# Performance work log

Hardware: AMD Instinct MI355X
Metric: run time of the kernel (lower is better)

Reference implementation:

```python
import jax, jax.numpy as jnp
import numpy as np

NEG_SLOPE = 0.2
EPS = 1e-16  # PyG softmax eps


def _gat_conv(x, src, dst, W, att_src, att_dst, bias, heads, out_ch):
    """PyG GATConv (eval mode, self-loops already appended, concat output)."""
    N = x.shape[0]
    xw = (x @ W).reshape(N, heads, out_ch)            # [N,H,C]
    a_src = jnp.sum(xw * att_src, axis=-1)            # [N,H]
    a_dst = jnp.sum(xw * att_dst, axis=-1)            # [N,H]
    e = jax.nn.leaky_relu(a_src[src] + a_dst[dst], NEG_SLOPE)  # [E,H]
    m = jax.ops.segment_max(e, dst, num_segments=N)   # [N,H] (self-loops -> no empty segs)
    e = jnp.exp(e - m[dst])
    denom = jax.ops.segment_sum(e, dst, num_segments=N)
    alpha = e / (denom[dst] + EPS)                    # [E,H]
    msg = xw[src] * alpha[:, :, None]                 # [E,H,C]
    out = jax.ops.segment_sum(msg, dst, num_segments=N)  # [N,H,C]
    return out.reshape(N, heads * out_ch) + bias


def setup_inputs() -> dict:
    key = jax.random.key(0)
    ks = jax.random.split(key, 12)
    N, E, F_in, H, C, NC = 20000, 320000, 512, 8, 64, 32
    x = jax.random.normal(ks[0], (N, F_in), dtype=jnp.float32)
    edge_index = jax.random.randint(ks[1], (2, E), 0, N, dtype=jnp.int64)
    g = lambda k, shape, fan: jax.random.normal(k, shape, dtype=jnp.float32) * (1.0 / np.sqrt(fan))
    return {
        "x": x,
        "edge_index": edge_index,
        "W1": g(ks[2], (F_in, H * C), F_in),
        "att_src1": g(ks[3], (H, C), C),
        "att_dst1": g(ks[4], (H, C), C),
        "b1": jnp.zeros((H * C,), dtype=jnp.float32),
        "W2": g(ks[5], (H * C, NC), H * C),
        "att_src2": g(ks[6], (1, NC), NC),
        "att_dst2": g(ks[7], (1, NC), NC),
        "b2": jnp.zeros((NC,), dtype=jnp.float32),
    }


def reference(x, edge_index, W1, att_src1, att_dst1, b1, W2, att_src2, att_dst2, b2):
    N = x.shape[0]
    H, C = att_src1.shape
    NC = att_src2.shape[1]
    # GATConv adds self-loops by default
    loops = jnp.arange(N, dtype=edge_index.dtype)
    src = jnp.concatenate([edge_index[0], loops])
    dst = jnp.concatenate([edge_index[1], loops])
    h = _gat_conv(x, src, dst, W1, att_src1, att_dst1, b1, H, C)
    h = jax.nn.elu(h)
    h = _gat_conv(h, src, dst, W2, att_src2, att_dst2, b2, 1, NC)
    return jax.nn.log_softmax(h, axis=1)
```

## Files before the change

kernel.cpp:

```cpp
#include <hip/hip_runtime.h>
#include <math.h>

#define NEG_SLOPE 0.2f
#define SM_EPS 1e-16f

typedef short short8 __attribute__((ext_vector_type(8)));
typedef float floatx4 __attribute__((ext_vector_type(4)));


__device__ inline unsigned short f2bf(float x) {
    unsigned int u = __float_as_uint(x);
    unsigned int r = (u + 0x7FFFu + ((u >> 16) & 1u)) >> 16;
    return (unsigned short)r;
}

__device__ inline float bf2f(unsigned short h) {
    return __uint_as_float(((unsigned int)h) << 16);
}

__device__ inline float bflo(unsigned int u) { return __uint_as_float(u << 16); }
__device__ inline float bfhi(unsigned int u) { return __uint_as_float(u & 0xFFFF0000u); }

__device__ inline float2 bf2x2(unsigned int u) {
    return make_float2(__uint_as_float(u << 16), __uint_as_float(u & 0xFFFF0000u));
}
__device__ inline float2 pk_fma(float w, float2 v, float2 a) {
    return make_float2(fmaf(w, v.x, a.x), fmaf(w, v.y, a.y));
}

__device__ __forceinline__ void gl_lds16(const unsigned short* g, unsigned short* l) {
    __builtin_amdgcn_global_load_lds(
        (const __attribute__((address_space(1))) unsigned int*)(g),
        (__attribute__((address_space(3))) unsigned int*)(l), 16, 0, 0);
}

__device__ inline void get_edge(const int* __restrict__ srcA, const int* __restrict__ dstA,
                                int e, int E, int& s, int& d) {
    if (e < E) { s = srcA[e]; d = dstA[e]; }
    else { s = e - E; d = e - E; }
}


__global__ __launch_bounds__(256) void k_prep(const float* __restrict__ x,
                                              unsigned short* __restrict__ xb,
                                              const float* __restrict__ W1,
                                              unsigned short* __restrict__ w1t,
                                              const float* __restrict__ W2,
                                              unsigned short* __restrict__ w2bt,
                                              const int* __restrict__ dstA,
                                              int E, int Ep,
                                              int* __restrict__ deg,
                                              int nblk_deg, int nblk_x) {
    __shared__ float tile[32][33];
    int bx = blockIdx.x;
    int t = threadIdx.x;
    if (bx < nblk_deg) {
        int e = bx * 256 + t;
        if (e < Ep) {
            int d = (e < E) ? dstA[e] : (e - E);
            atomicAdd(&deg[d], 1);
        }
    } else if (bx < nblk_deg + nblk_x) {
        int i = ((bx - nblk_deg) * 256 + t) * 4;
        float4 v = *(const float4*)(x + i);
        ushort4 o;
        o.x = f2bf(v.x); o.y = f2bf(v.y); o.z = f2bf(v.z); o.w = f2bf(v.w);
        *(ushort4*)(xb + i) = o;
    } else if (bx < nblk_deg + nblk_x + 256) {
        int b = bx - nblk_deg - nblk_x;
        int kb = (b & 15) * 32;
        int nb = (b >> 4) * 32;
        int tx = t & 31, ty = t >> 5;
        #pragma unroll
        for (int i = 0; i < 32; i += 8)
            tile[ty + i][tx] = W1[(size_t)(kb + ty + i) * 512 + nb + tx];
        __syncthreads();
        #pragma unroll
        for (int i = 0; i < 32; i += 8)
            w1t[(size_t)(nb + ty + i) * 512 + kb + tx] = f2bf(tile[tx][ty + i]);
    } else {
        int i = (bx - nblk_deg - nblk_x - 256) * 256 + t;
        int c = i >> 9, k = i & 511;
        w2bt[i] = f2bf(W2[k * 32 + c]);
    }
}


__global__ __launch_bounds__(256) void k_scan_fused(const int* __restrict__ deg,
                                                    int* __restrict__ part,
                                                    int* __restrict__ done,
                                                    int* __restrict__ off,
                                                    int* __restrict__ cursor,
                                                    int N, int nblk) {
    __shared__ int sm[256];
    int bx = blockIdx.x, t = threadIdx.x;
    int i = bx * 256 + t;
    int v = (i < N) ? deg[i] : 0;
    sm[t] = v; __syncthreads();
    for (int o = 1; o < 256; o <<= 1) {
        int x = (t >= o) ? sm[t - o] : 0;
        __syncthreads();
        sm[t] += x;
        __syncthreads();
    }
    int incl_v = sm[t];
    if (t == 255) {
        part[bx] = sm[255];
        __threadfence();
        atomicAdd(done, 1);
    }
    if (t == 0) {
        while (atomicAdd(done, 0) < nblk) { }
        __threadfence();
    }
    __syncthreads();
    int partial = 0;
    for (int j = t; j < bx; j += 256) partial += atomicAdd(&part[j], 0);
    sm[t] = partial; __syncthreads();
    for (int o = 128; o > 0; o >>= 1) {
        if (t < o) sm[t] += sm[t + o];
        __syncthreads();
    }
    int base = sm[0];
    if (i < N) {
        int vv = incl_v + base;
        off[i + 1] = vv;
        cursor[i] = vv - v;
        if (i == 0) off[0] = 0;
    }
}

__global__ __launch_bounds__(256) void k_scatter(const int* __restrict__ srcA, const int* __restrict__ dstA,
                                                 int E, int Ep, int* __restrict__ cursor,
                                                 int* __restrict__ src_s) {
    int e = blockIdx.x * 256 + threadIdx.x;
    if (e >= Ep) return;
    int s, d; get_edge(srcA, dstA, e, E, s, d);
    int p = atomicAdd(&cursor[d], 1);
    src_s[p] = s;
}


__global__ __launch_bounds__(256, 4) void k_gemm1_mfma(const unsigned short* __restrict__ A,
                                                       const unsigned short* __restrict__ Bt,
                                                       const float* __restrict__ att_s,
                                                       const float* __restrict__ att_d,
                                                       unsigned short* __restrict__ C,
                                                       float* __restrict__ a_sd,
                                                       float* __restrict__ a_dd, int M) {
    const int K = 512;
    __shared__ unsigned short As[2][64 * 32];
    __shared__ unsigned short Bs[2][128 * 32];
    int t = threadIdx.x;
    int lane = t & 63;
    int w = t >> 6;
    int row0 = blockIdx.x * 64;
    int col0 = blockIdx.y * 128;
    int wm = (w >> 1) * 32, wn = (w & 1) * 64;
    int l15 = lane & 15, q = lane >> 4;

    int srl = lane >> 2;
    int sgc = ((lane & 3) ^ ((lane >> 3) & 3)) * 8;

    floatx4 acc[2][4] = {};

    auto STAGE = [&](int buf, int k0) {
        gl_lds16(A  + (size_t)(row0 + w * 16 + srl) * K + k0 + sgc, &As[buf][(w * 16) * 32]);
        gl_lds16(Bt + (size_t)(col0 + w * 32 + srl) * K + k0 + sgc, &Bs[buf][(w * 32) * 32]);
        gl_lds16(Bt + (size_t)(col0 + w * 32 + 16 + srl) * K + k0 + sgc, &Bs[buf][(w * 32 + 16) * 32]);
    };

    STAGE(0, 0);
    asm volatile("s_waitcnt vmcnt(0)" ::: "memory");
    __builtin_amdgcn_s_barrier();

    int swz = (l15 >> 1) & 3;
    int buf = 0;
    for (int k0 = 0; k0 < K; k0 += 32) {
        if (k0 + 32 < K) {
            STAGE(buf ^ 1, k0 + 32);
            asm volatile("s_waitcnt vmcnt(3)" ::: "memory");
        } else {
            asm volatile("s_waitcnt vmcnt(0)" ::: "memory");
        }
        __builtin_amdgcn_s_barrier();
        __builtin_amdgcn_sched_barrier(0);
        short8 af[2], bfr[4];
        int sw = (q ^ swz) << 3;
        #pragma unroll
        for (int i = 0; i < 2; ++i)
            af[i] = *(const short8*)(&As[buf][(wm + i * 16 + l15) * 32 + sw]);
        #pragma unroll
        for (int j = 0; j < 4; ++j)
            bfr[j] = *(const short8*)(&Bs[buf][(wn + j * 16 + l15) * 32 + sw]);
        #pragma unroll
        for (int i = 0; i < 2; ++i)
            #pragma unroll
            for (int j = 0; j < 4; ++j)
                acc[i][j] = __builtin_amdgcn_mfma_f32_16x16x32_bf16(af[i], bfr[j], acc[i][j], 0, 0, 0);
        asm volatile("s_waitcnt lgkmcnt(0)" ::: "memory");
        __builtin_amdgcn_sched_barrier(0);
        __builtin_amdgcn_s_barrier();
        buf ^= 1;
    }

    #pragma unroll
    for (int i = 0; i < 2; ++i) {
        #pragma unroll
        for (int p = 0; p < 4; ++p) {
            int r = row0 + wm + i * 16 + q * 4 + p;
            if (r < M) {
                #pragma unroll
                for (int j = 0; j < 4; ++j) {
                    int c = col0 + wn + j * 16 + l15;
                    C[(size_t)r * 512 + c] = f2bf(acc[i][j][p]);
                }
            }
        }
    }

    int hh = blockIdx.y * 2 + (w & 1);
    float asr[4], adr[4];
    #pragma unroll
    for (int j = 0; j < 4; ++j) {
        asr[j] = att_s[hh * 64 + j * 16 + l15];
        adr[j] = att_d[hh * 64 + j * 16 + l15];
    }
    #pragma unroll
    for (int i = 0; i < 2; ++i) {
        #pragma unroll
        for (int p = 0; p < 4; ++p) {
            float ds = 0.f, dd = 0.f;
            #pragma unroll
            for (int j = 0; j < 4; ++j) {
                ds = fmaf(acc[i][j][p], asr[j], ds);
                dd = fmaf(acc[i][j][p], adr[j], dd);
            }
            #pragma unroll
            for (int mk = 1; mk <= 8; mk <<= 1) {
                ds += __shfl_xor(ds, mk);
                dd += __shfl_xor(dd, mk);
            }
            int r = row0 + wm + i * 16 + q * 4 + p;
            if (l15 == 0 && r < M) {
                a_sd[(size_t)hh * M + r] = ds;
                a_dd[(size_t)hh * M + r] = dd;
            }
        }
    }
}


__global__ __launch_bounds__(256) void k_l1(const unsigned short* __restrict__ xw,
                                            const float* __restrict__ a_s,
                                            const float* __restrict__ a_d,
                                            const int* __restrict__ off,
                                            const int* __restrict__ src_s,
                                            const float* __restrict__ bias,
                                            unsigned short* __restrict__ hout, int N) {
    int wid = threadIdx.x >> 6, lane = threadIdx.x & 63;
    int h = blockIdx.x & 7;
    int n = (blockIdx.x >> 3) * 32 + wid * 8 + (lane >> 3);
    int li = lane & 7;
    if (n >= N) return;
    int p0 = off[n], p1 = off[n + 1];
    const float* ash = a_s + (size_t)h * N;
    float adv = a_d[(size_t)h * N + n];
    const size_t cbase = (size_t)h * 64 + (size_t)li * 8;

    float2 acc[4] = {};
    float s = 0.f;
    int p = p0;
    if (p + 4 <= p1) {
        int s0 = src_s[p], s1 = src_s[p + 1], s2 = src_s[p + 2], s3 = src_s[p + 3];
        while (true) {
            const uint4 u0 = *(const uint4*)(xw + (size_t)s0 * 512 + cbase);
            const uint4 u1 = *(const uint4*)(xw + (size_t)s1 * 512 + cbase);
            const uint4 u2 = *(const uint4*)(xw + (size_t)s2 * 512 + cbase);
            const uint4 u3 = *(const uint4*)(xw + (size_t)s3 * 512 + cbase);
            float e0 = ash[s0] + adv; e0 = e0 > 0.f ? e0 : NEG_SLOPE * e0;
            float e1 = ash[s1] + adv; e1 = e1 > 0.f ? e1 : NEG_SLOPE * e1;
            float e2 = ash[s2] + adv; e2 = e2 > 0.f ? e2 : NEG_SLOPE * e2;
            float e3 = ash[s3] + adv; e3 = e3 > 0.f ? e3 : NEG_SLOPE * e3;
            int np = p + 4;
            bool more = (np + 4 <= p1);
            int t0 = 0, t1 = 0, t2 = 0, t3 = 0;
            if (more) {
                t0 = src_s[np]; t1 = src_s[np + 1];
                t2 = src_s[np + 2]; t3 = src_s[np + 3];
            }
            float w0 = __expf(e0);
            float w1 = __expf(e1);
            float w2 = __expf(e2);
            float w3 = __expf(e3);
            s += (w0 + w1) + (w2 + w3);
            acc[0] = pk_fma(w0, bf2x2(u0.x), acc[0]);
            acc[1] = pk_fma(w0, bf2x2(u0.y), acc[1]);
            acc[2] = pk_fma(w0, bf2x2(u0.z), acc[2]);
            acc[3] = pk_fma(w0, bf2x2(u0.w), acc[3]);
            acc[0] = pk_fma(w1, bf2x2(u1.x), acc[0]);
            acc[1] = pk_fma(w1, bf2x2(u1.y), acc[1]);
            acc[2] = pk_fma(w1, bf2x2(u1.z), acc[2]);
            acc[3] = pk_fma(w1, bf2x2(u1.w), acc[3]);
            acc[0] = pk_fma(w2, bf2x2(u2.x), acc[0]);
            acc[1] = pk_fma(w2, bf2x2(u2.y), acc[1]);
            acc[2] = pk_fma(w2, bf2x2(u2.z), acc[2]);
            acc[3] = pk_fma(w2, bf2x2(u2.w), acc[3]);
            acc[0] = pk_fma(w3, bf2x2(u3.x), acc[0]);
            acc[1] = pk_fma(w3, bf2x2(u3.y), acc[1]);
            acc[2] = pk_fma(w3, bf2x2(u3.z), acc[2]);
            acc[3] = pk_fma(w3, bf2x2(u3.w), acc[3]);
            p = np;
            if (!more) break;
            s0 = t0; s1 = t1; s2 = t2; s3 = t3;
        }
    }
    for (; p < p1; ++p) {
        int s0 = src_s[p];
        const uint4 u0 = *(const uint4*)(xw + (size_t)s0 * 512 + cbase);
        float e0 = ash[s0] + adv; e0 = e0 > 0.f ? e0 : NEG_SLOPE * e0;
        float w0 = __expf(e0);
        s += w0;
        acc[0] = pk_fma(w0, bf2x2(u0.x), acc[0]);
        acc[1] = pk_fma(w0, bf2x2(u0.y), acc[1]);
        acc[2] = pk_fma(w0, bf2x2(u0.z), acc[2]);
        acc[3] = pk_fma(w0, bf2x2(u0.w), acc[3]);
    }

    float inv = 1.f / (s + SM_EPS);
    unsigned int ov[4];
    #pragma unroll
    for (int j = 0; j < 4; ++j) {
        float v0 = acc[j].x * inv + bias[cbase + 2 * j];
        float v1 = acc[j].y * inv + bias[cbase + 2 * j + 1];
        v0 = v0 > 0.f ? v0 : __expf(v0) - 1.f;
        v1 = v1 > 0.f ? v1 : __expf(v1) - 1.f;
        ov[j] = (unsigned int)f2bf(v0) | ((unsigned int)f2bf(v1) << 16);
    }
    *(uint4*)(hout + (size_t)n * 512 + cbase) = make_uint4(ov[0], ov[1], ov[2], ov[3]);
}


__global__ __launch_bounds__(256) void k_gemm2_mfma(const unsigned short* __restrict__ A,
                                                    const unsigned short* __restrict__ Bt,
                                                    const float* __restrict__ att_s,
                                                    const float* __restrict__ att_d,
                                                    unsigned short* __restrict__ O,
                                                    float* __restrict__ a_s, float* __restrict__ a_d,
                                                    int M) {
    const int K = 512;
    __shared__ unsigned short As[64 * 512];
    __shared__ unsigned short Bs[32 * 512];
    int t = threadIdx.x;
    int lane = t & 63;
    int w = t >> 6;
    int row0 = blockIdx.x * 64;
    int l15 = lane & 15, q = lane >> 4;

    #pragma unroll
    for (int i = 0; i < 16; ++i) {
        int r = w * 16 + i;
        gl_lds16(A + (size_t)(row0 + r) * K + ((lane ^ (r & 7)) << 3), &As[r * 512]);
    }
    #pragma unroll
    for (int i = 0; i < 8; ++i) {
        int r = w * 8 + i;
        gl_lds16(Bt + (size_t)r * K + ((lane ^ (r & 7)) << 3), &Bs[r * 512]);
    }
    __syncthreads();

    floatx4 acc[2] = {};
    int ra = w * 16 + l15;
    int rb0 = l15, rb1 = 16 + l15;
    #pragma unroll
    for (int k0 = 0; k0 < K; k0 += 32) {
        int cc = (k0 >> 3) + q;
        short8 af = *(const short8*)(&As[ra * 512 + ((cc ^ (ra & 7)) << 3)]);
        short8 b0 = *(const short8*)(&Bs[rb0 * 512 + ((cc ^ (rb0 & 7)) << 3)]);
        short8 b1 = *(const short8*)(&Bs[rb1 * 512 + ((cc ^ (rb1 & 7)) << 3)]);
        acc[0] = __builtin_amdgcn_mfma_f32_16x16x32_bf16(af, b0, acc[0], 0, 0, 0);
        acc[1] = __builtin_amdgcn_mfma_f32_16x16x32_bf16(af, b1, acc[1], 0, 0, 0);
    }

    float as_lo = att_s[l15], as_hi = att_s[16 + l15];
    float ad_lo = att_d[l15], ad_hi = att_d[16 + l15];
    #pragma unroll
    for (int p = 0; p < 4; ++p) {
        int r = row0 + w * 16 + q * 4 + p;
        bool ok = r < M;
        float v0 = acc[0][p], v1 = acc[1][p];
        if (ok) {
            O[(size_t)r * 32 + l15]      = f2bf(v0);
            O[(size_t)r * 32 + 16 + l15] = f2bf(v1);
        }
        float ds = v0 * as_lo + v1 * as_hi;
        float dd = v0 * ad_lo + v1 * ad_hi;
        #pragma unroll
        for (int mk = 1; mk <= 8; mk <<= 1) {
            ds += __shfl_xor(ds, mk);
            dd += __shfl_xor(dd, mk);
        }
        if (ok && l15 == 0) { a_s[r] = ds; a_d[r] = dd; }
    }
}


__global__ __launch_bounds__(256) void k_l2(const unsigned short* __restrict__ hw2,
                                            const float* __restrict__ a_s,
                                            const float* __restrict__ a_d,
                                            const int* __restrict__ off,
                                            const int* __restrict__ src_s,
                                            const float* __restrict__ bias,
                                            float* __restrict__ outp, int N) {
    int wid = threadIdx.x >> 6, lane = threadIdx.x & 63;
    int n = blockIdx.x * 4 + wid;
    if (n >= N) return;
    int p0 = off[n], p1 = off[n + 1];
    float adv = a_d[n];
    int e8 = lane >> 3;
    int li = lane & 7;
    const int cbase = li * 4;

    float acc[4] = {};
    float s = 0.f;
    int p = p0;
    for (; p + 16 <= p1; p += 16) {
        int sA = src_s[p + e8];
        int sB = src_s[p + 8 + e8];
        const uint2 uA = *(const uint2*)(hw2 + (size_t)sA * 32 + cbase);
        const uint2 uB = *(const uint2*)(hw2 + (size_t)sB * 32 + cbase);
        float eA = a_s[sA] + adv; eA = eA > 0.f ? eA : NEG_SLOPE * eA;
        float eB = a_s[sB] + adv; eB = eB > 0.f ? eB : NEG_SLOPE * eB;
        float wA = __expf(eA);
        float wB = __expf(eB);
        s += wA + wB;
        acc[0] = fmaf(wA, bflo(uA.x), acc[0]); acc[1] = fmaf(wA, bfhi(uA.x), acc[1]);
        acc[2] = fmaf(wA, bflo(uA.y), acc[2]); acc[3] = fmaf(wA, bfhi(uA.y), acc[3]);
        acc[0] = fmaf(wB, bflo(uB.x), acc[0]); acc[1] = fmaf(wB, bfhi(uB.x), acc[1]);
        acc[2] = fmaf(wB, bflo(uB.y), acc[2]); acc[3] = fmaf(wB, bfhi(uB.y), acc[3]);
    }
    for (; p + 8 <= p1; p += 8) {
        int sA = src_s[p + e8];
        const uint2 uA = *(const uint2*)(hw2 + (size_t)sA * 32 + cbase);
        float eA = a_s[sA] + adv; eA = eA > 0.f ? eA : NEG_SLOPE * eA;
        float wA = __expf(eA);
        s += wA;
        acc[0] = fmaf(wA, bflo(uA.x), acc[0]); acc[1] = fmaf(wA, bfhi(uA.x), acc[1]);
        acc[2] = fmaf(wA, bflo(uA.y), acc[2]); acc[3] = fmaf(wA, bfhi(uA.y), acc[3]);
    }
    if (p < p1) {
        int nb = p1 - p;
        bool val = e8 < nb;
        int sA = src_s[val ? p + e8 : p];
        const uint2 uA = *(const uint2*)(hw2 + (size_t)sA * 32 + cbase);
        float eA = a_s[sA] + adv; eA = eA > 0.f ? eA : NEG_SLOPE * eA;
        float wA = val ? __expf(eA) : 0.f;
        s += wA;
        acc[0] = fmaf(wA, bflo(uA.x), acc[0]); acc[1] = fmaf(wA, bfhi(uA.x), acc[1]);
        acc[2] = fmaf(wA, bflo(uA.y), acc[2]); acc[3] = fmaf(wA, bfhi(uA.y), acc[3]);
    }

    #pragma unroll
    for (int mk = 8; mk <= 32; mk <<= 1) {
        s += __shfl_xor(s, mk);
        #pragma unroll
        for (int j = 0; j < 4; ++j) acc[j] += __shfl_xor(acc[j], mk);
    }

    float inv = 1.f / (s + SM_EPS);
    float v[4];
    #pragma unroll
    for (int j = 0; j < 4; ++j) v[j] = acc[j] * inv + bias[cbase + j];

    float mx = fmaxf(fmaxf(v[0], v[1]), fmaxf(v[2], v[3]));
    mx = fmaxf(mx, __shfl_xor(mx, 1));
    mx = fmaxf(mx, __shfl_xor(mx, 2));
    mx = fmaxf(mx, __shfl_xor(mx, 4));
    float sum = 0.f;
    #pragma unroll
    for (int j = 0; j < 4; ++j) sum += __expf(v[j] - mx);
    sum += __shfl_xor(sum, 1);
    sum += __shfl_xor(sum, 2);
    sum += __shfl_xor(sum, 4);
    float lse = __logf(sum);
    if (e8 == 0) {
        float4 o = make_float4(v[0] - mx - lse, v[1] - mx - lse,
                               v[2] - mx - lse, v[3] - mx - lse);
        *(float4*)(outp + (size_t)n * 32 + cbase) = o;
    }
}


extern "C" void kernel_launch(void* const* d_in, const int* in_sizes, int n_in,
                              void* d_out, int out_size, void* d_ws, size_t ws_size,
                              hipStream_t stream) {
    const float* x   = (const float*)d_in[0];
    const int*   ei  = (const int*)d_in[1];
    const float* W1  = (const float*)d_in[2];
    const float* as1 = (const float*)d_in[3];
    const float* ad1 = (const float*)d_in[4];
    const float* b1  = (const float*)d_in[5];
    const float* W2  = (const float*)d_in[6];
    const float* as2 = (const float*)d_in[7];
    const float* ad2 = (const float*)d_in[8];
    const float* b2  = (const float*)d_in[9];
    float* out = (float*)d_out;

    const int F = 512;
    const int N = in_sizes[0] / F;
    const int E = in_sizes[1] / 2;
    const int Ep = E + N;
    const int* srcA = ei;
    const int* dstA = ei + E;

    char* w = (char*)d_ws;
    auto alloc = [&](size_t b) -> void* {
        void* p = (void*)w;
        w += (b + 255) & ~(size_t)255;
        return p;
    };
    unsigned short* xbf  = (unsigned short*)alloc((size_t)N * 512 * 2);
    unsigned short* w1t  = (unsigned short*)alloc((size_t)512 * 512 * 2);
    unsigned short* w2bt = (unsigned short*)alloc((size_t)32 * 512 * 2);
    unsigned short* xw1  = (unsigned short*)alloc((size_t)N * 512 * 2);
    unsigned short* hbuf = (unsigned short*)alloc((size_t)N * 512 * 2);
    float* a_s1 = (float*)alloc((size_t)N * 8 * 4);
    float* a_d1 = (float*)alloc((size_t)N * 8 * 4);
    unsigned short* hw2 = (unsigned short*)alloc((size_t)N * 32 * 2);
    float* a_s2 = (float*)alloc((size_t)N * 4);
    float* a_d2 = (float*)alloc((size_t)N * 4);
    int* deg    = (int*)alloc((size_t)N * 4);
    int* done   = (int*)alloc(256);
    int* incl   = (int*)alloc((size_t)N * 4);
    int* part   = (int*)alloc(256 * 4);
    int* off    = (int*)alloc((size_t)(N + 1) * 4);
    int* cursor = (int*)alloc((size_t)N * 4);
    int* src_s  = (int*)alloc((size_t)Ep * 4);
    (void)incl;

    int egrid = (Ep + 255) / 256;
    int sgrid = (N + 255) / 256;
    int ngrid4 = (N + 3) / 4;
    int nblk_x = (N * 512 / 4) / 256;
    int nblk_w2 = (32 * 512 + 255) / 256;

    hipMemsetAsync(deg, 0, (((size_t)N * 4 + 255) & ~(size_t)255) + 256, stream);

    k_prep<<<egrid + nblk_x + 256 + nblk_w2, 256, 0, stream>>>(
        x, xbf, W1, w1t, W2, w2bt, dstA, E, Ep, deg, egrid, nblk_x);

    k_scan_fused<<<sgrid, 256, 0, stream>>>(deg, part, done, off, cursor, N, sgrid);
    k_scatter<<<egrid, 256, 0, stream>>>(srcA, dstA, E, Ep, cursor, src_s);

    {
        dim3 g1((N + 63) / 64, 512 / 128);
        k_gemm1_mfma<<<g1, 256, 0, stream>>>(xbf, w1t, as1, ad1, xw1, a_s1, a_d1, N);
    }
    {
        int ngrid32 = (N + 31) / 32;
        k_l1<<<ngrid32 * 8, 256, 0, stream>>>(xw1, a_s1, a_d1, off, src_s, b1, hbuf, N);
    }

    k_gemm2_mfma<<<(N + 63) / 64, 256, 0, stream>>>(hbuf, w2bt, as2, ad2, hw2, a_s2, a_d2, N);
    k_l2<<<ngrid4, 256, 0, stream>>>(hw2, a_s2, a_d2, off, src_s, b2, out, N);
}
```

Measured before the change: 222.1 us.

## Precompute layer-1 edge softmax weights in scatter, store fp16 xw, byte-offset indices

The CSR scatter kernel now runs after GEMM1 and computes exp(leaky_relu(a_s+a_d)) for all 8 heads per edge into a sorted weight buffer. The layer-1 aggregation then streams these weights instead of gathering a_s per source and evaluating exp. Source indices are stored pre-shifted as byte offsets so both aggregation kernels skip the multiply. The GEMM1 output switches from bf16 to fp16 for extra mantissa precision. In exchange, the scatter now does 16 random gathers per edge and writes an extra Ep*8 float buffer, and fp16 can overflow on large activations.

```diff
diff --git a/kernel.cpp b/kernel.cpp
--- a/kernel.cpp
+++ b/kernel.cpp
@@ -1,4 +1,5 @@
 #include <hip/hip_runtime.h>
+#include <hip/hip_fp16.h>
 #include <math.h>
 
 #define NEG_SLOPE 0.2f
@@ -21,11 +22,13 @@
 __device__ inline float bflo(unsigned int u) { return __uint_as_float(u << 16); }
 __device__ inline float bfhi(unsigned int u) { return __uint_as_float(u & 0xFFFF0000u); }
 
-__device__ inline float2 bf2x2(unsigned int u) {
-    return make_float2(__uint_as_float(u << 16), __uint_as_float(u & 0xFFFF0000u));
-}
-__device__ inline float2 pk_fma(float w, float2 v, float2 a) {
-    return make_float2(fmaf(w, v.x, a.x), fmaf(w, v.y, a.y));
+__device__ inline void fma8h(float w, const uint4& u, float2 acc[4]) {
+    const __half2* hp = reinterpret_cast<const __half2*>(&u);
+    #pragma unroll
+    for (int k = 0; k < 4; ++k) {
+        acc[k].x = fmaf(w, __half2float(__low2half(hp[k])), acc[k].x);
+        acc[k].y = fmaf(w, __half2float(__high2half(hp[k])), acc[k].y);
+    }
 }
 
 __device__ __forceinline__ void gl_lds16(const unsigned short* g, unsigned short* l) {
@@ -130,14 +133,26 @@
     }
 }
 
-__global__ __launch_bounds__(256) void k_scatter(const int* __restrict__ srcA, const int* __restrict__ dstA,
-                                                 int E, int Ep, int* __restrict__ cursor,
-                                                 int* __restrict__ src_s) {
+
+__global__ __launch_bounds__(256) void k_scatterw(const int* __restrict__ srcA,
+                                                  const int* __restrict__ dstA,
+                                                  int E, int Ep, int N,
+                                                  int* __restrict__ cursor,
+                                                  int* __restrict__ src_b,
+                                                  const float* __restrict__ a_s1,
+                                                  const float* __restrict__ a_d1,
+                                                  float* __restrict__ wbuf) {
     int e = blockIdx.x * 256 + threadIdx.x;
     if (e >= Ep) return;
     int s, d; get_edge(srcA, dstA, e, E, s, d);
     int p = atomicAdd(&cursor[d], 1);
-    src_s[p] = s;
+    src_b[p] = s << 10;
+    #pragma unroll
+    for (int h = 0; h < 8; ++h) {
+        float ev = a_s1[(size_t)h * N + s] + a_d1[(size_t)h * N + d];
+        ev = ev > 0.f ? ev : NEG_SLOPE * ev;
+        wbuf[(size_t)h * Ep + p] = __expf(ev);
+    }
 }
 
 
@@ -213,18 +228,19 @@
                 #pragma unroll
                 for (int j = 0; j < 4; ++j) {
                     int c = col0 + wn + j * 16 + l15;
-                    C[(size_t)r * 512 + c] = f2bf(acc[i][j][p]);
+                    __half hh = __float2half(acc[i][j][p]);
+                    C[(size_t)r * 512 + c] = reinterpret_cast<unsigned short&>(hh);
                 }
             }
         }
     }
 
-    int hh = blockIdx.y * 2 + (w & 1);
+    int hh2 = blockIdx.y * 2 + (w & 1);
     float asr[4], adr[4];
     #pragma unroll
     for (int j = 0; j < 4; ++j) {
-        asr[j] = att_s[hh * 64 + j * 16 + l15];
-        adr[j] = att_d[hh * 64 + j * 16 + l15];
+        asr[j] = att_s[hh2 * 64 + j * 16 + l15];
+        adr[j] = att_d[hh2 * 64 + j * 16 + l15];
     }
     #pragma unroll
     for (int i = 0; i < 2; ++i) {
@@ -243,8 +259,8 @@
             }
             int r = row0 + wm + i * 16 + q * 4 + p;
             if (l15 == 0 && r < M) {
-                a_sd[(size_t)hh * M + r] = ds;
-                a_dd[(size_t)hh * M + r] = dd;
+                a_sd[(size_t)hh2 * M + r] = ds;
+                a_dd[(size_t)hh2 * M + r] = dd;
             }
         }
     }
@@ -252,79 +268,56 @@
 
 
 __global__ __launch_bounds__(256) void k_l1(const unsigned short* __restrict__ xw,
-                                            const float* __restrict__ a_s,
-                                            const float* __restrict__ a_d,
+                                            const float* __restrict__ wbuf,
                                             const int* __restrict__ off,
-                                            const int* __restrict__ src_s,
+                                            const int* __restrict__ src_b,
                                             const float* __restrict__ bias,
-                                            unsigned short* __restrict__ hout, int N) {
+                                            unsigned short* __restrict__ hout,
+                                            int N, int Ep) {
     int wid = threadIdx.x >> 6, lane = threadIdx.x & 63;
     int h = blockIdx.x & 7;
     int n = (blockIdx.x >> 3) * 32 + wid * 8 + (lane >> 3);
     int li = lane & 7;
     if (n >= N) return;
     int p0 = off[n], p1 = off[n + 1];
-    const float* ash = a_s + (size_t)h * N;
-    float adv = a_d[(size_t)h * N + n];
+    const float* wh = wbuf + (size_t)h * Ep;
+    const char* xbase = (const char*)xw + h * 128 + li * 16;
     const size_t cbase = (size_t)h * 64 + (size_t)li * 8;
 
     float2 acc[4] = {};
     float s = 0.f;
     int p = p0;
     if (p + 4 <= p1) {
-        int s0 = src_s[p], s1 = src_s[p + 1], s2 = src_s[p + 2], s3 = src_s[p + 3];
+        int o0 = src_b[p], o1 = src_b[p + 1], o2 = src_b[p + 2], o3 = src_b[p + 3];
         while (true) {
-            const uint4 u0 = *(const uint4*)(xw + (size_t)s0 * 512 + cbase);
-            const uint4 u1 = *(const uint4*)(xw + (size_t)s1 * 512 + cbase);
-            const uint4 u2 = *(const uint4*)(xw + (size_t)s2 * 512 + cbase);
-            const uint4 u3 = *(const uint4*)(xw + (size_t)s3 * 512 + cbase);
-            float e0 = ash[s0] + adv; e0 = e0 > 0.f ? e0 : NEG_SLOPE * e0;
-            float e1 = ash[s1] + adv; e1 = e1 > 0.f ? e1 : NEG_SLOPE * e1;
-            float e2 = ash[s2] + adv; e2 = e2 > 0.f ? e2 : NEG_SLOPE * e2;
-            float e3 = ash[s3] + adv; e3 = e3 > 0.f ? e3 : NEG_SLOPE * e3;
+            const uint4 u0 = *(const uint4*)(xbase + o0);
+            const uint4 u1 = *(const uint4*)(xbase + o1);
+            const uint4 u2 = *(const uint4*)(xbase + o2);
+            const uint4 u3 = *(const uint4*)(xbase + o3);
+            float w0 = wh[p], w1 = wh[p + 1], w2 = wh[p + 2], w3 = wh[p + 3];
             int np = p + 4;
             bool more = (np + 4 <= p1);
             int t0 = 0, t1 = 0, t2 = 0, t3 = 0;
             if (more) {
-                t0 = src_s[np]; t1 = src_s[np + 1];
-                t2 = src_s[np + 2]; t3 = src_s[np + 3];
+                t0 = src_b[np]; t1 = src_b[np + 1];
+                t2 = src_b[np + 2]; t3 = src_b[np + 3];
             }
-            float w0 = __expf(e0);
-            float w1 = __expf(e1);
-            float w2 = __expf(e2);
-            float w3 = __expf(e3);
             s += (w0 + w1) + (w2 + w3);
-            acc[0] = pk_fma(w0, bf2x2(u0.x), acc[0]);
-            acc[1] = pk_fma(w0, bf2x2(u0.y), acc[1]);
-            acc[2] = pk_fma(w0, bf2x2(u0.z), acc[2]);
-            acc[3] = pk_fma(w0, bf2x2(u0.w), acc[3]);
-            acc[0] = pk_fma(w1, bf2x2(u1.x), acc[0]);
-            acc[1] = pk_fma(w1, bf2x2(u1.y), acc[1]);
-            acc[2] = pk_fma(w1, bf2x2(u1.z), acc[2]);
-            acc[3] = pk_fma(w1, bf2x2(u1.w), acc[3]);
-            acc[0] = pk_fma(w2, bf2x2(u2.x), acc[0]);
-            acc[1] = pk_fma(w2, bf2x2(u2.y), acc[1]);
-            acc[2] = pk_fma(w2, bf2x2(u2.z), acc[2]);
-            acc[3] = pk_fma(w2, bf2x2(u2.w), acc[3]);
-            acc[0] = pk_fma(w3, bf2x2(u3.x), acc[0]);
-            acc[1] = pk_fma(w3, bf2x2(u3.y), acc[1]);
-            acc[2] = pk_fma(w3, bf2x2(u3.z), acc[2]);
-            acc[3] = pk_fma(w3, bf2x2(u3.w), acc[3]);
+            fma8h(w0, u0, acc);
+            fma8h(w1, u1, acc);
+            fma8h(w2, u2, acc);
+            fma8h(w3, u3, acc);
             p = np;
             if (!more) break;
-            s0 = t0; s1 = t1; s2 = t2; s3 = t3;
+            o0 = t0; o1 = t1; o2 = t2; o3 = t3;
         }
     }
     for (; p < p1; ++p) {
-        int s0 = src_s[p];
-        const uint4 u0 = *(const uint4*)(xw + (size_t)s0 * 512 + cbase);
-        float e0 = ash[s0] + adv; e0 = e0 > 0.f ? e0 : NEG_SLOPE * e0;
-        float w0 = __expf(e0);
+        int o0 = src_b[p];
+        const uint4 u0 = *(const uint4*)(xbase + o0);
+        float w0 = wh[p];
         s += w0;
-        acc[0] = pk_fma(w0, bf2x2(u0.x), acc[0]);
-        acc[1] = pk_fma(w0, bf2x2(u0.y), acc[1]);
-        acc[2] = pk_fma(w0, bf2x2(u0.z), acc[2]);
-        acc[3] = pk_fma(w0, bf2x2(u0.w), acc[3]);
+        fma8h(w0, u0, acc);
     }
 
     float inv = 1.f / (s + SM_EPS);
@@ -409,7 +402,7 @@
                                             const float* __restrict__ a_s,
                                             const float* __restrict__ a_d,
                                             const int* __restrict__ off,
-                                            const int* __restrict__ src_s,
+                                            const int* __restrict__ src_b,
                                             const float* __restrict__ bias,
                                             float* __restrict__ outp, int N) {
     int wid = threadIdx.x >> 6, lane = threadIdx.x & 63;
@@ -420,17 +413,19 @@
     int e8 = lane >> 3;
     int li = lane & 7;
     const int cbase = li * 4;
+    const char* hb = (const char*)hw2 + cbase * 2;
+    const char* ab = (const char*)a_s;
 
     float acc[4] = {};
     float s = 0.f;
     int p = p0;
     for (; p + 16 <= p1; p += 16) {
-        int sA = src_s[p + e8];
-        int sB = src_s[p + 8 + e8];
-        const uint2 uA = *(const uint2*)(hw2 + (size_t)sA * 32 + cbase);
-        const uint2 uB = *(const uint2*)(hw2 + (size_t)sB * 32 + cbase);
-        float eA = a_s[sA] + adv; eA = eA > 0.f ? eA : NEG_SLOPE * eA;
-        float eB = a_s[sB] + adv; eB = eB > 0.f ? eB : NEG_SLOPE * eB;
+        int oA = src_b[p + e8];
+        int oB = src_b[p + 8 + e8];
+        const uint2 uA = *(const uint2*)(hb + (oA >> 4));
+        const uint2 uB = *(const uint2*)(hb + (oB >> 4));
+        float eA = *(const float*)(ab + (oA >> 8)) + adv; eA = eA > 0.f ? eA : NEG_SLOPE * eA;
+        float eB = *(const float*)(ab + (oB >> 8)) + adv; eB = eB > 0.f ? eB : NEG_SLOPE * eB;
         float wA = __expf(eA);
         float wB = __expf(eB);
         s += wA + wB;
@@ -440,9 +435,9 @@
         acc[2] = fmaf(wB, bflo(uB.y), acc[2]); acc[3] = fmaf(wB, bfhi(uB.y), acc[3]);
     }
     for (; p + 8 <= p1; p += 8) {
-        int sA = src_s[p + e8];
-        const uint2 uA = *(const uint2*)(hw2 + (size_t)sA * 32 + cbase);
-        float eA = a_s[sA] + adv; eA = eA > 0.f ? eA : NEG_SLOPE * eA;
+        int oA = src_b[p + e8];
+        const uint2 uA = *(const uint2*)(hb + (oA >> 4));
+        float eA = *(const float*)(ab + (oA >> 8)) + adv; eA = eA > 0.f ? eA : NEG_SLOPE * eA;
         float wA = __expf(eA);
         s += wA;
         acc[0] = fmaf(wA, bflo(uA.x), acc[0]); acc[1] = fmaf(wA, bfhi(uA.x), acc[1]);
@@ -451,9 +446,9 @@
     if (p < p1) {
         int nb = p1 - p;
         bool val = e8 < nb;
-        int sA = src_s[val ? p + e8 : p];
-        const uint2 uA = *(const uint2*)(hw2 + (size_t)sA * 32 + cbase);
-        float eA = a_s[sA] + adv; eA = eA > 0.f ? eA : NEG_SLOPE * eA;
+        int oA = src_b[val ? p + e8 : p];
+        const uint2 uA = *(const uint2*)(hb + (oA >> 4));
+        float eA = *(const float*)(ab + (oA >> 8)) + adv; eA = eA > 0.f ? eA : NEG_SLOPE * eA;
         float wA = val ? __expf(eA) : 0.f;
         s += wA;
         acc[0] = fmaf(wA, bflo(uA.x), acc[0]); acc[1] = fmaf(wA, bfhi(uA.x), acc[1]);
@@ -531,12 +526,11 @@
     float* a_d2 = (float*)alloc((size_t)N * 4);
     int* deg    = (int*)alloc((size_t)N * 4);
     int* done   = (int*)alloc(256);
-    int* incl   = (int*)alloc((size_t)N * 4);
     int* part   = (int*)alloc(256 * 4);
     int* off    = (int*)alloc((size_t)(N + 1) * 4);
     int* cursor = (int*)alloc((size_t)N * 4);
-    int* src_s  = (int*)alloc((size_t)Ep * 4);
-    (void)incl;
+    int* src_b  = (int*)alloc((size_t)Ep * 4);
+    float* wbuf = (float*)alloc((size_t)Ep * 8 * 4);
 
     int egrid = (Ep + 255) / 256;
     int sgrid = (N + 255) / 256;
@@ -549,18 +543,20 @@
     k_prep<<<egrid + nblk_x + 256 + nblk_w2, 256, 0, stream>>>(
         x, xbf, W1, w1t, W2, w2bt, dstA, E, Ep, deg, egrid, nblk_x);
 
-    k_scan_fused<<<sgrid, 256, 0, stream>>>(deg, part, done, off, cursor, N, sgrid);
-    k_scatter<<<egrid, 256, 0, stream>>>(srcA, dstA, E, Ep, cursor, src_s);
-
     {
         dim3 g1((N + 63) / 64, 512 / 128);
         k_gemm1_mfma<<<g1, 256, 0, stream>>>(xbf, w1t, as1, ad1, xw1, a_s1, a_d1, N);
     }
+
+    k_scan_fused<<<sgrid, 256, 0, stream>>>(deg, part, done, off, cursor, N, sgrid);
+    k_scatterw<<<egrid, 256, 0, stream>>>(srcA, dstA, E, Ep, N, cursor, src_b,
+                                          a_s1, a_d1, wbuf);
+
     {
         int ngrid32 = (N + 31) / 32;
-        k_l1<<<ngrid32 * 8, 256, 0, stream>>>(xw1, a_s1, a_d1, off, src_s, b1, hbuf, N);
+        k_l1<<<ngrid32 * 8, 256, 0, stream>>>(xw1, wbuf, off, src_b, b1, hbuf, N, Ep);
     }
 
     k_gemm2_mfma<<<(N + 63) / 64, 256, 0, stream>>>(hbuf, w2bt, as2, ad2, hw2, a_s2, a_d2, N);
-    k_l2<<<ngrid4, 256, 0, stream>>>(hw2, a_s2, a_d2, off, src_s, b2, out, N);
-}
+    k_l2<<<ngrid4, 256, 0, stream>>>(hw2, a_s2, a_d2, off, src_b, b2, out, N);
+}
```

Measured after the change: 254.3 us. +14.5%, slower.

## Enlarge layer-1 GEMM tile to 128x128 with 64-wide K steps and XOR swizzle

Applied to the files above, without the earlier changes.

Retiles the first-layer bf16 MFMA GEMM from 64x128 to 128x128 block tiles. K advances 64 per stage, each wave holds a 4x4 accumulator grid, and the LDS layout uses a new 8-way XOR swizzle. The goal is more operand reuse per LDS load and fewer barriers per K pass. In exchange it uses more LDS and registers, drops the occupancy hint, and waits for the prefetch only at the end of each step, which may weaken overlap. An unused workspace allocation is also removed.

```diff
diff --git a/kernel.cpp b/kernel.cpp
--- a/kernel.cpp
+++ b/kernel.cpp
@@ -141,71 +141,69 @@
 }
 
 
-__global__ __launch_bounds__(256, 4) void k_gemm1_mfma(const unsigned short* __restrict__ A,
-                                                       const unsigned short* __restrict__ Bt,
-                                                       const float* __restrict__ att_s,
-                                                       const float* __restrict__ att_d,
-                                                       unsigned short* __restrict__ C,
-                                                       float* __restrict__ a_sd,
-                                                       float* __restrict__ a_dd, int M) {
+__global__ __launch_bounds__(256) void k_gemm1_mfma(const unsigned short* __restrict__ A,
+                                                    const unsigned short* __restrict__ Bt,
+                                                    const float* __restrict__ att_s,
+                                                    const float* __restrict__ att_d,
+                                                    unsigned short* __restrict__ C,
+                                                    float* __restrict__ a_sd,
+                                                    float* __restrict__ a_dd, int M) {
     const int K = 512;
-    __shared__ unsigned short As[2][64 * 32];
-    __shared__ unsigned short Bs[2][128 * 32];
+    __shared__ unsigned short As[2][128 * 64];
+    __shared__ unsigned short Bs[2][128 * 64];
     int t = threadIdx.x;
     int lane = t & 63;
     int w = t >> 6;
-    int row0 = blockIdx.x * 64;
+    int row0 = blockIdx.x * 128;
     int col0 = blockIdx.y * 128;
-    int wm = (w >> 1) * 32, wn = (w & 1) * 64;
+    int wm = (w >> 1) * 64, wn = (w & 1) * 64;
     int l15 = lane & 15, q = lane >> 4;
 
-    int srl = lane >> 2;
-    int sgc = ((lane & 3) ^ ((lane >> 3) & 3)) * 8;
-
-    floatx4 acc[2][4] = {};
+    int r8 = lane >> 3;
+    int sgc = ((lane & 7) ^ r8) * 8;
+    int srow = w * 32 + r8;
+
+    floatx4 acc[4][4] = {};
 
     auto STAGE = [&](int buf, int k0) {
-        gl_lds16(A  + (size_t)(row0 + w * 16 + srl) * K + k0 + sgc, &As[buf][(w * 16) * 32]);
-        gl_lds16(Bt + (size_t)(col0 + w * 32 + srl) * K + k0 + sgc, &Bs[buf][(w * 32) * 32]);
-        gl_lds16(Bt + (size_t)(col0 + w * 32 + 16 + srl) * K + k0 + sgc, &Bs[buf][(w * 32 + 16) * 32]);
+        #pragma unroll
+        for (int i = 0; i < 4; ++i) {
+            gl_lds16(A  + (size_t)(row0 + srow + i * 8) * K + k0 + sgc, &As[buf][(w * 32 + i * 8) * 64]);
+            gl_lds16(Bt + (size_t)(col0 + srow + i * 8) * K + k0 + sgc, &Bs[buf][(w * 32 + i * 8) * 64]);
+        }
     };
 
     STAGE(0, 0);
     asm volatile("s_waitcnt vmcnt(0)" ::: "memory");
     __builtin_amdgcn_s_barrier();
 
-    int swz = (l15 >> 1) & 3;
     int buf = 0;
-    for (int k0 = 0; k0 < K; k0 += 32) {
-        if (k0 + 32 < K) {
-            STAGE(buf ^ 1, k0 + 32);
-            asm volatile("s_waitcnt vmcnt(3)" ::: "memory");
-        } else {
-            asm volatile("s_waitcnt vmcnt(0)" ::: "memory");
-        }
-        __builtin_amdgcn_s_barrier();
-        __builtin_amdgcn_sched_barrier(0);
-        short8 af[2], bfr[4];
-        int sw = (q ^ swz) << 3;
-        #pragma unroll
-        for (int i = 0; i < 2; ++i)
-            af[i] = *(const short8*)(&As[buf][(wm + i * 16 + l15) * 32 + sw]);
-        #pragma unroll
-        for (int j = 0; j < 4; ++j)
-            bfr[j] = *(const short8*)(&Bs[buf][(wn + j * 16 + l15) * 32 + sw]);
-        #pragma unroll
-        for (int i = 0; i < 2; ++i)
+    for (int k0 = 0; k0 < K; k0 += 64) {
+        if (k0 + 64 < K) STAGE(buf ^ 1, k0 + 64);
+        #pragma unroll
+        for (int ks = 0; ks < 2; ++ks) {
+            short8 af[4], bfr[4];
+            int sw = (((ks * 4 + q) ^ (l15 & 7))) * 8;
+            #pragma unroll
+            for (int i = 0; i < 4; ++i)
+                af[i] = *(const short8*)(&As[buf][(wm + i * 16 + l15) * 64 + sw]);
             #pragma unroll
             for (int j = 0; j < 4; ++j)
-                acc[i][j] = __builtin_amdgcn_mfma_f32_16x16x32_bf16(af[i], bfr[j], acc[i][j], 0, 0, 0);
-        asm volatile("s_waitcnt lgkmcnt(0)" ::: "memory");
+                bfr[j] = *(const short8*)(&Bs[buf][(wn + j * 16 + l15) * 64 + sw]);
+            #pragma unroll
+            for (int i = 0; i < 4; ++i)
+                #pragma unroll
+                for (int j = 0; j < 4; ++j)
+                    acc[i][j] = __builtin_amdgcn_mfma_f32_16x16x32_bf16(af[i], bfr[j], acc[i][j], 0, 0, 0);
+        }
+        asm volatile("s_waitcnt vmcnt(0) lgkmcnt(0)" ::: "memory");
         __builtin_amdgcn_sched_barrier(0);
         __builtin_amdgcn_s_barrier();
         buf ^= 1;
     }
 
     #pragma unroll
-    for (int i = 0; i < 2; ++i) {
+    for (int i = 0; i < 4; ++i) {
         #pragma unroll
         for (int p = 0; p < 4; ++p) {
             int r = row0 + wm + i * 16 + q * 4 + p;
@@ -227,7 +225,7 @@
         adr[j] = att_d[hh * 64 + j * 16 + l15];
     }
     #pragma unroll
-    for (int i = 0; i < 2; ++i) {
+    for (int i = 0; i < 4; ++i) {
         #pragma unroll
         for (int p = 0; p < 4; ++p) {
             float ds = 0.f, dd = 0.f;
@@ -531,12 +529,10 @@
     float* a_d2 = (float*)alloc((size_t)N * 4);
     int* deg    = (int*)alloc((size_t)N * 4);
     int* done   = (int*)alloc(256);
-    int* incl   = (int*)alloc((size_t)N * 4);
     int* part   = (int*)alloc(256 * 4);
     int* off    = (int*)alloc((size_t)(N + 1) * 4);
     int* cursor = (int*)alloc((size_t)N * 4);
     int* src_s  = (int*)alloc((size_t)Ep * 4);
-    (void)incl;
 
     int egrid = (Ep + 255) / 256;
     int sgrid = (N + 255) / 256;
@@ -553,7 +549,7 @@
     k_scatter<<<egrid, 256, 0, stream>>>(srcA, dstA, E, Ep, cursor, src_s);
 
     {
-        dim3 g1((N + 63) / 64, 512 / 128);
+        dim3 g1((N + 127) / 128, 512 / 128);
         k_gemm1_mfma<<<g1, 256, 0, stream>>>(xbf, w1t, as1, ad1, xw1, a_s1, a_d1, N);
     }
     {
```

Result: slower. 229.0 us (+3.1%).
